# Performance work log

Measured on AMD Instinct MI355X. Metric: run time of the kernel, lower is better.

The kernel has to match this reference:

```python
import jax, jax.numpy as jnp
import numpy as np

N, E, IN_DIM, H, OUT, MAPD = 20000, 640000, 24, 128, 24, 512
SLOPE = 0.01  # torch F.leaky_relu default


def setup_inputs() -> dict:
    key = jax.random.key(0)
    ks = jax.random.split(key, 20)
    g = lambda i, shape, s: jax.random.normal(ks[i], shape, jnp.float32) * s
    inp = {
        "feats": g(0, (N, IN_DIM), 1.0),
        "e_w": jax.random.uniform(ks[1], (E, 1), dtype=jnp.float32),
        "maps_embedding": g(2, (N, MAPD), 1.0),
        "snorm_n": jnp.ones((N, 1), jnp.float32),
        "src": jax.random.randint(ks[3], (E,), 0, N),
        "dst": jax.random.randint(ks[4], (E,), 0, N),
        "W_eh": g(5, (H, IN_DIM), (2.0 / IN_DIM) ** 0.5), "b_eh": jnp.zeros((H,), jnp.float32),
        "W_ee": g(6, (H, 1), 1.0), "b_ee": jnp.zeros((H,), jnp.float32),
        "W_cat": g(7, (H, H + MAPD), (2.0 / (H + MAPD)) ** 0.5), "b_cat": jnp.zeros((H,), jnp.float32),
        "Ws1": g(8, (H, H), (2.0 / H) ** 0.5), "Wf1": g(9, (H, H), (2.0 / H) ** 0.5),
        "a1": g(10, (2 * H,), (2.0 / (2 * H)) ** 0.5),
        "Ws2": g(11, (H, H), (2.0 / H) ** 0.5), "Wf2": g(12, (H, H), (2.0 / H) ** 0.5),
        "a2": g(13, (2 * H,), (2.0 / (2 * H)) ** 0.5),
        "W_out": g(14, (OUT, H), (2.0 / H) ** 0.5), "b_out": jnp.zeros((OUT,), jnp.float32),
    }
    return inp


def gat_layer(h, src, dst, Ws, Wf, a):
    # My_GATLayer with (as constructed in My_GAT) relu=False, att_ew=False, dropouts=0.
    h_in = h
    h_s = h @ Ws.T                         # [N,H] self transform
    z = h @ Wf.T                           # [N,H] message transform
    # attention score = leaky_relu(a^T [z_src, z_dst]) computed via per-node halves
    s_src = z @ a[:H]                      # [N]
    s_dst = z @ a[H:]                      # [N]
    e = jax.nn.leaky_relu(s_src[src] + s_dst[dst], SLOPE)          # [E]
    # numerically stable segment softmax over incoming edges grouped by dst
    m = jax.ops.segment_max(e, dst, num_segments=N)
    m = jnp.where(jnp.isfinite(m), m, 0.0)
    ex = jnp.exp(e - m[dst])
    denom = jax.ops.segment_sum(ex, dst, num_segments=N)
    alpha = ex / jnp.maximum(denom[dst], 1e-16)                    # [E]
    agg = jax.ops.segment_sum(alpha[:, None] * z[src], dst, num_segments=N)  # [N,H]
    indeg = jax.ops.segment_sum(jnp.ones_like(e), dst, num_segments=N)
    # DGL update_all leaves zero-in-degree nodes at their prior ndata['h'] (= h_in)
    h_node = jnp.where(indeg[:, None] > 0, h_s + agg, h_in)
    return h_in + h_node                   # residual connection; relu disabled (positional-arg bug)


def reference(feats, e_w, maps_embedding, snorm_n, src, dst,
              W_eh, b_eh, W_ee, b_ee, W_cat, b_cat,
              Ws1, Wf1, a1, Ws2, Wf2, a2, W_out, b_out):
    feats = feats.reshape(feats.shape[0], -1)
    h = feats @ W_eh.T + b_eh                                  # embedding_h
    _e = e_w @ W_ee.T + b_ee                                   # edge embedding (stored on g.edata['w'], unused since att_ew binds to attn_drop)
    h = jnp.concatenate([maps_embedding, h], axis=-1) @ W_cat.T + b_cat
    h = jax.nn.relu(h)
    h = gat_layer(h, src, dst, Ws1, Wf1, a1)
    h = gat_layer(h, src, dst, Ws2, Wf2, a2)
    return h @ W_out.T + b_out
```

## Files before the change

kernel.cpp:

```cpp
#include <hip/hip_runtime.h>

#define HBLK 128
#define EPB 4096

typedef __attribute__((ext_vector_type(8))) short s8v;
typedef __attribute__((ext_vector_type(4))) float f32x4;
typedef __attribute__((ext_vector_type(8))) _Float16 h8f;

__device__ inline void split2(float x, short& h, short& l) {
    unsigned hb = __float_as_uint(x) & 0xFFFF0000u;
    float hf = __uint_as_float(hb);
    float lf = x - hf;
    h = (short)(hb >> 16);
    l = (short)(__float_as_uint(lf) >> 16);
}

__device__ inline void split8(const float4& a0, const float4& a1, s8v& ah, s8v& al) {
    float vv[8];
    *(float4*)&vv[0] = a0;
    *(float4*)&vv[4] = a1;
#pragma unroll
    for (int e = 0; e < 8; ++e) {
        short hh, ll;
        split2(vv[e], hh, ll);
        ah[e] = hh;
        al[e] = ll;
    }
}


__global__ void hist_pack(const int* __restrict__ dst, int* __restrict__ histT,
                          int E, int NB1,
                          const float* __restrict__ W0, const float* __restrict__ W1,
                          const float* __restrict__ W2, const float* __restrict__ W3,
                          short* __restrict__ dh, short* __restrict__ dl,
                          const float* __restrict__ Wcat, int ldw, int mapd,
                          const float* __restrict__ Weh, int indim,
                          const float* __restrict__ beh, const float* __restrict__ bcat,
                          short* __restrict__ ch,
                          float* __restrict__ bcomb, int K) {
    __shared__ int h[256];
    const int y = blockIdx.y;
    const int t = threadIdx.x;
    if (y == 0) {
        const int blk = blockIdx.x;
        if (blk >= NB1) return;
        h[t] = 0;
        __syncthreads();
        const int e0 = blk * EPB;
        const int e1 = min(E, e0 + EPB);
        for (int e = e0 + t; e < e1; e += 256)
            atomicAdd(&h[dst[e] >> 7], 1);
        __syncthreads();
        histT[t * NB1 + blk] = h[t];
    } else if (y < 5) {
        if (blockIdx.x >= 64) return;
        const int m = y - 1;
        const long i = (long)blockIdx.x * 256 + t;
        const float* Ws[4] = {W0, W1, W2, W3};
        const int c = (int)(i >> 7), k = (int)(i & 127);
        float x = Ws[m][c * HBLK + k];
        short hh, ll;
        split2(x, hh, ll);
        const int j = c >> 4, l16 = c & 15;
        const int chunk = k >> 5, quad = (k >> 3) & 3, tt = k & 7;
        const long off = (long)m * 16384 + (((long)(chunk * 8 + j) * 64) + quad * 16 + l16) * 8 + tt;
        dh[off] = hh;
        dl[off] = ll;
    } else {
        const long i = (long)blockIdx.x * 256 + t;
        const long total = (long)HBLK * K;
        if (i < total) {
            const int c = (int)(i / K), k = (int)(i % K);
            float x = 0.f;
            if (k < mapd) {
                x = Wcat[(long)c * ldw + k];
            } else if (k < mapd + indim) {
                const float* wc = Wcat + (long)c * ldw + mapd;
                const int kk = k - mapd;
                float s = 0.f;
                for (int j = 0; j < HBLK; ++j) s += wc[j] * Weh[j * indim + kk];
                x = s;
            }
            short hh, ll;
            split2(x, hh, ll);
            const int j = c >> 4, l16 = c & 15;
            const int chunk = k >> 5, quad = (k >> 3) & 3, tt = k & 7;
            const long off = (((long)(chunk * 8 + j) * 64) + quad * 16 + l16) * 8 + tt;
            ch[off] = hh;
        } else if (i < total + HBLK) {
            const int c = (int)(i - total);
            const float* wc = Wcat + (long)c * ldw + mapd;
            float s = bcat[c];
            for (int j = 0; j < HBLK; ++j) s += wc[j] * beh[j];
            bcomb[c] = s;
        }
    }
}

__global__ void scan1(const int* __restrict__ counts, int* __restrict__ offs,
                      int* __restrict__ bsums, int n) {
    __shared__ int lds[256];
    const int t = threadIdx.x;
    const int i = blockIdx.x * 256 + t;
    const int v = (i < n) ? counts[i] : 0;
    lds[t] = v;
    __syncthreads();
    for (int off = 1; off < 256; off <<= 1) {
        int add = (t >= off) ? lds[t - off] : 0;
        __syncthreads();
        lds[t] += add;
        __syncthreads();
    }
    if (i < n) offs[i] = lds[t] - v;
    if (t == 255) bsums[blockIdx.x] = lds[255];
}

__device__ inline void local_bsum_scan(const int* __restrict__ bsums, int nb,
                                       int* bex, int* tmp) {
    const int t = threadIdx.x;
    const int v = (t < nb) ? bsums[t] : 0;
    tmp[t] = v;
    __syncthreads();
    for (int off = 1; off < 256; off <<= 1) {
        int add = (t >= off) ? tmp[t - off] : 0;
        __syncthreads();
        tmp[t] += add;
        __syncthreads();
    }
    bex[t] = tmp[t] - v;
    __syncthreads();
}

__global__ void bin_scatter(const int* __restrict__ src, const int* __restrict__ dst,
                            const int* __restrict__ histT, const int* __restrict__ bsums,
                            int* __restrict__ ebuf, int E, int NB1) {
    __shared__ int cur[256];
    __shared__ int bex[256];
    __shared__ int tmp[256];
    const int t = threadIdx.x, blk = blockIdx.x;
    local_bsum_scan(bsums, NB1, bex, tmp);
    const int li = t * NB1 + blk;
    cur[t] = histT[li] + bex[li >> 8];
    __syncthreads();
    const int e0 = blk * EPB;
    const int e1 = min(E, e0 + EPB);
    for (int e = e0 + t; e < e1; e += 256) {
        const int d = dst[e];
        const int p = atomicAdd(&cur[d >> 7], 1);
        ebuf[p] = (src[e] << 7) | (d & 127);
    }
}

__global__ void bucket_sort(const int* __restrict__ ebuf, const int* __restrict__ histT,
                            const int* __restrict__ bsums,
                            int* __restrict__ offs, int* __restrict__ srcs,
                            int N, int E, int NB1) {
    __shared__ int cnt[256];
    __shared__ int cur[256];
    __shared__ int bex[256];
    const int t = threadIdx.x, b = blockIdx.x;
    local_bsum_scan(bsums, NB1, bex, cnt);
    const int li0 = b * NB1;
    const int ebase = histT[li0] + bex[li0 >> 8];
    int eend = E;
    if (b + 1 < 256) {
        const int li1 = (b + 1) * NB1;
        eend = histT[li1] + bex[li1 >> 8];
    }
    cnt[t] = 0;
    __syncthreads();
    for (int e = ebase + t; e < eend; e += 256)
        atomicAdd(&cnt[ebuf[e] & 127], 1);
    __syncthreads();
    const int own = cnt[t];
    for (int off = 1; off < 256; off <<= 1) {
        int add = (t >= off) ? cnt[t - off] : 0;
        __syncthreads();
        cnt[t] += add;
        __syncthreads();
    }
    const int excl = cnt[t] - own;
    cur[t] = ebase + excl;
    const int node = (b << 7) + t;
    if (t < 128 && node < N) offs[node] = ebase + excl;
    if (b == 0 && t == 0) offs[N] = E;
    __syncthreads();
    for (int e = ebase + t; e < eend; e += 256) {
        const int ed = ebuf[e];
        const int p = atomicAdd(&cur[ed & 127], 1);
        srcs[p] = ed >> 7;
    }
}

__global__ __launch_bounds__(128, 2) void gemm_bigk(
    const float* __restrict__ A1, int lda1, int K1,
    const float* __restrict__ A2, int lda2, int Kin,
    int K,
    const short* __restrict__ Wh,
    const float* __restrict__ bias,
    float* __restrict__ Cf, int M)
{
    __shared__ short lds_h[2][4096];
    const int tid = threadIdx.x;
    const int wv = tid >> 6;
    const int lane = tid & 63;
    const int l16 = lane & 15;
    const int quad = lane >> 4;
    const int m0 = blockIdx.x * 32 + wv * 16;
    int ra = m0 + l16;
    if (ra >= M) ra = M - 1;
    const long r1 = (long)ra * lda1;
    const long r2 = (long)ra * lda2;
    const int NC = K >> 5;

    f32x4 acc[8];
#pragma unroll
    for (int j = 0; j < 8; ++j) acc[j] = (f32x4){0.f, 0.f, 0.f, 0.f};

#define LOAD_A(d0, d1, kb)                                      \
    {                                                           \
        const int col0 = (kb) + quad * 8;                       \
        if (col0 < K1) {                                        \
            const float* ap = A1 + r1 + col0;                   \
            d0 = *(const float4*)ap;                            \
            d1 = *(const float4*)(ap + 4);                      \
        } else if (col0 < Kin) {                                \
            const float* ap = A2 + r2 + (col0 - K1);            \
            d0 = *(const float4*)ap;                            \
            d1 = *(const float4*)(ap + 4);                      \
        } else {                                                \
            d0 = make_float4(0.f, 0.f, 0.f, 0.f);               \
            d1 = make_float4(0.f, 0.f, 0.f, 0.f);               \
        }                                                       \
    }
#define LOAD_W(c)                                               \
    {                                                           \
        const int4* gh = (const int4*)(Wh + (long)(c) * 4096);  \
        wh0 = gh[tid * 4];     wh1 = gh[tid * 4 + 1];           \
        wh2 = gh[tid * 4 + 2]; wh3 = gh[tid * 4 + 3];           \
    }
#define WRITE_W(b)                                              \
    {                                                           \
        int4* bh = (int4*)lds_h[b];                             \
        bh[tid * 4] = wh0;     bh[tid * 4 + 1] = wh1;           \
        bh[tid * 4 + 2] = wh2; bh[tid * 4 + 3] = wh3;           \
    }

    int4 wh0, wh1, wh2, wh3;
    LOAD_W(0)
    WRITE_W(0)
    LOAD_W(1)
    float4 a0c, a1c, a0n, a1n, a0p, a1p;
    float4 a0q = make_float4(0.f, 0.f, 0.f, 0.f);
    float4 a1q = make_float4(0.f, 0.f, 0.f, 0.f);
    LOAD_A(a0c, a1c, 0)
    LOAD_A(a0n, a1n, 32)
    LOAD_A(a0p, a1p, 64)
    asm volatile("s_waitcnt lgkmcnt(0)" ::: "memory");
    __builtin_amdgcn_s_barrier();
    asm volatile("" ::: "memory");

    for (int c = 0; c < NC; ++c) {
        const int nb = c & 1;
        if (c + 3 < NC) {
            LOAD_A(a0q, a1q, (c + 3) * 32)
        }
        s8v ah, al;
        split8(a0c, a1c, ah, al);
#pragma unroll
        for (int j = 0; j < 8; ++j) {
            const s8v whf = *(const s8v*)&lds_h[nb][(j * 64 + lane) * 8];
            acc[j] = __builtin_amdgcn_mfma_f32_16x16x32_bf16(ah, whf, acc[j], 0, 0, 0);
            acc[j] = __builtin_amdgcn_mfma_f32_16x16x32_bf16(al, whf, acc[j], 0, 0, 0);
        }
        if (c + 1 < NC) {
            WRITE_W(nb ^ 1)
            if (c + 2 < NC) LOAD_W(c + 2)
            asm volatile("s_waitcnt lgkmcnt(0)" ::: "memory");
            __builtin_amdgcn_s_barrier();
            asm volatile("" ::: "memory");
        }
        a0c = a0n; a1c = a1n;
        a0n = a0p; a1n = a1p;
        a0p = a0q; a1p = a1q;
    }
#undef LOAD_A
#undef LOAD_W
#undef WRITE_W

#pragma unroll
    for (int r = 0; r < 4; ++r) {
        const int gr = m0 + quad * 4 + r;
        if (gr >= M) continue;
#pragma unroll
        for (int j = 0; j < 8; ++j) {
            const int col = j * 16 + l16;
            float v = acc[j][r] + bias[col];
            Cf[(long)gr * HBLK + col] = fmaxf(v, 0.f);
        }
    }
}

__global__ __launch_bounds__(256, 2) void gemm_layer(
    const float* __restrict__ A,
    const short* __restrict__ Wsh,
    const short* __restrict__ Wfh, const short* __restrict__ Wfl,
    float* __restrict__ hsOut, _Float16* __restrict__ zOut,
    const float* __restrict__ avec,
    float* __restrict__ sOut, float* __restrict__ dOut, int M)
{
    __shared__ short lh[16384];
    __shared__ short ll[16384];
    const int tid = threadIdx.x;
    const int wv = tid >> 6;
    const int lane = tid & 63;
    const int l16 = lane & 15;
    const int quad = lane >> 4;
    const int m0 = blockIdx.x * 64 + wv * 16;
    int ra = m0 + l16;
    if (ra >= M) ra = M - 1;
    const float* arow = A + (long)ra * HBLK + quad * 8;

    {
        const int4* gh = (const int4*)Wfh;
        const int4* gl = (const int4*)Wfl;
        int4* bh = (int4*)lh;
        int4* bl = (int4*)ll;
#pragma unroll
        for (int i = 0; i < 8; ++i) {
            bh[i * 256 + tid] = gh[i * 256 + tid];
            bl[i * 256 + tid] = gl[i * 256 + tid];
        }
    }
    float4 aw0[4], aw1[4];
#pragma unroll
    for (int c = 0; c < 4; ++c) {
        aw0[c] = *(const float4*)(arow + c * 32);
        aw1[c] = *(const float4*)(arow + c * 32 + 4);
    }
    int4 wsh[8];
    {
        const int4* gh = (const int4*)Wsh;
#pragma unroll
        for (int i = 0; i < 8; ++i) wsh[i] = gh[i * 256 + tid];
    }
    s8v ahf[4], alf[4];
#pragma unroll
    for (int c = 0; c < 4; ++c) split8(aw0[c], aw1[c], ahf[c], alf[c]);

    f32x4 acc[8];
#pragma unroll
    for (int j = 0; j < 8; ++j) acc[j] = (f32x4){0.f, 0.f, 0.f, 0.f};
    asm volatile("s_waitcnt lgkmcnt(0)" ::: "memory");
    __builtin_amdgcn_s_barrier();
    asm volatile("" ::: "memory");

#pragma unroll
    for (int c = 0; c < 4; ++c) {
#pragma unroll
        for (int j = 0; j < 8; ++j) {
            const s8v whf = *(const s8v*)&lh[((c * 8 + j) * 64 + lane) * 8];
            const s8v wlf = *(const s8v*)&ll[((c * 8 + j) * 64 + lane) * 8];
            acc[j] = __builtin_amdgcn_mfma_f32_16x16x32_bf16(ahf[c], whf, acc[j], 0, 0, 0);
            acc[j] = __builtin_amdgcn_mfma_f32_16x16x32_bf16(ahf[c], wlf, acc[j], 0, 0, 0);
            acc[j] = __builtin_amdgcn_mfma_f32_16x16x32_bf16(alf[c], whf, acc[j], 0, 0, 0);
        }
    }
#pragma unroll
    for (int r = 0; r < 4; ++r) {
        const int gr = m0 + quad * 4 + r;
        if (gr >= M) continue;
#pragma unroll
        for (int j = 0; j < 8; ++j)
            zOut[(long)gr * HBLK + j * 16 + l16] = (_Float16)acc[j][r];
    }
    {
        float av0[8], av1[8];
#pragma unroll
        for (int j = 0; j < 8; ++j) {
            av0[j] = avec[j * 16 + l16];
            av1[j] = avec[128 + j * 16 + l16];
        }
#pragma unroll
        for (int r = 0; r < 4; ++r) {
            float ssp = 0.f, sdp = 0.f;
#pragma unroll
            for (int j = 0; j < 8; ++j) {
                const float v = acc[j][r];
                ssp += v * av0[j];
                sdp += v * av1[j];
            }
#pragma unroll
            for (int off = 1; off < 16; off <<= 1) {
                ssp += __shfl_xor(ssp, off);
                sdp += __shfl_xor(sdp, off);
            }
            const int gr = m0 + quad * 4 + r;
            if (l16 == 0 && gr < M) {
                sOut[gr] = ssp;
                dOut[gr] = sdp;
            }
        }
    }

    asm volatile("s_waitcnt lgkmcnt(0)" ::: "memory");
    __builtin_amdgcn_s_barrier();
    asm volatile("" ::: "memory");
    {
        int4* bh = (int4*)lh;
#pragma unroll
        for (int i = 0; i < 8; ++i) bh[i * 256 + tid] = wsh[i];
    }
    asm volatile("s_waitcnt lgkmcnt(0)" ::: "memory");
    __builtin_amdgcn_s_barrier();
    asm volatile("" ::: "memory");

#pragma unroll
    for (int j = 0; j < 8; ++j) acc[j] = (f32x4){0.f, 0.f, 0.f, 0.f};
#pragma unroll
    for (int c = 0; c < 4; ++c) {
#pragma unroll
        for (int j = 0; j < 8; ++j) {
            const s8v whf = *(const s8v*)&lh[((c * 8 + j) * 64 + lane) * 8];
            acc[j] = __builtin_amdgcn_mfma_f32_16x16x32_bf16(ahf[c], whf, acc[j], 0, 0, 0);
            acc[j] = __builtin_amdgcn_mfma_f32_16x16x32_bf16(alf[c], whf, acc[j], 0, 0, 0);
        }
    }
#pragma unroll
    for (int r = 0; r < 4; ++r) {
        const int gr = m0 + quad * 4 + r;
        if (gr >= M) continue;
#pragma unroll
        for (int j = 0; j < 8; ++j)
            hsOut[(long)gr * HBLK + j * 16 + l16] = acc[j][r];
    }
}

template <int FOUT>
__global__ void gat_gather(const float* __restrict__ h_in, const float* __restrict__ hs,
                           const _Float16* __restrict__ zh,
                           const float* __restrict__ s_src, const float* __restrict__ s_dst,
                           const int* __restrict__ offs, const int* __restrict__ srcs,
                           float* __restrict__ h_out,
                           const float* __restrict__ Wout, const float* __restrict__ bout,
                           float* __restrict__ outp, int OUTD, int N) {
    __shared__ float wlds[FOUT ? (32 * 132 + 4 * 132) : 4];
    const int tid = threadIdx.x;
    const int wave = tid >> 6;
    const int lane = tid & 63;
    if constexpr (FOUT) {
        for (int i = tid; i < OUTD * HBLK; i += 256)
            wlds[(i >> 7) * 132 + (i & 127)] = Wout[i];
        __syncthreads();
    }
    const int n = blockIdx.x * 4 + wave;
    if (n >= N) return;
    const int g = lane >> 4, l = lane & 15;
    const int beg = offs[n], end = offs[n + 1];
    const int deg = end - beg;
    const float sd = s_dst[n];

    const long base = (long)n * HBLK + 8 * l;
    float4 hi0, hi1, hv0, hv1;
    if (g == 0) {
        hi0 = *(const float4*)(h_in + base);
        hi1 = *(const float4*)(h_in + base + 4);
        if (deg > 0) {
            hv0 = *(const float4*)(hs + base);
            hv1 = *(const float4*)(hs + base + 4);
        }
    }
    float bo = 0.f;
    if constexpr (FOUT) {
        if (lane < OUTD) bo = bout[lane];
    }

    float acc[8] = {};
    if (deg > 0) {
        if (deg <= 64) {
            const int sA = srcs[beg + min(lane, deg - 1)];
            float e = sd + s_src[sA];
            e = e > 0.f ? e : 0.01f * e;
            if (lane >= deg) e = -INFINITY;
            float mv = e;
#pragma unroll
            for (int off = 32; off; off >>= 1) mv = fmaxf(mv, __shfl_xor(mv, off));
            const float ex = (lane < deg) ? __expf(e - mv) : 0.f;
            float sv = ex;
#pragma unroll
            for (int off = 32; off; off >>= 1) sv += __shfl_xor(sv, off);
            const float w = ex / fmaxf(sv, 1e-16f);

            const int nK = (deg + 3) >> 2;
            int k = 0;
            for (; k + 1 < nK; k += 2) {
                const int i0 = 4 * k + g;
                const int i1 = i0 + 4;
                const int s0 = __shfl(sA, i0);
                const int s1 = __shfl(sA, i1);
                const float w0 = __shfl(w, i0);
                const float w1 = __shfl(w, i1);
                const h8f z0 = *(const h8f*)(zh + (long)s0 * HBLK + 8 * l);
                const h8f z1 = *(const h8f*)(zh + (long)s1 * HBLK + 8 * l);
#pragma unroll
                for (int e2 = 0; e2 < 8; ++e2)
                    acc[e2] += w0 * (float)z0[e2] + w1 * (float)z1[e2];
            }
            if (k < nK) {
                const int i0 = 4 * k + g;
                const int s0 = __shfl(sA, i0);
                const float w0 = __shfl(w, i0);
                const h8f z0 = *(const h8f*)(zh + (long)s0 * HBLK + 8 * l);
#pragma unroll
                for (int e2 = 0; e2 < 8; ++e2)
                    acc[e2] += w0 * (float)z0[e2];
            }
        } else {
            float m = -INFINITY, s = 0.f;
            for (int i = beg + lane; i < end; i += 64) {
                float e = sd + s_src[srcs[i]];
                e = e > 0.f ? e : 0.01f * e;
                float nm = fmaxf(m, e);
                s = s * __expf(m - nm) + __expf(e - nm);
                m = nm;
            }
#pragma unroll
            for (int off = 32; off > 0; off >>= 1) {
                float m2 = __shfl_down(m, off);
                float s2 = __shfl_down(s, off);
                if (m2 > m) {
                    float t = m; m = m2; m2 = t;
                    float ts = s; s = s2; s2 = ts;
                }
                s = (m == -INFINITY) ? 0.f : s + s2 * __expf(m2 - m);
            }
            m = __shfl(m, 0);
            s = __shfl(s, 0);
            const float inv = 1.f / fmaxf(s, 1e-16f);
            for (int i = beg + g; i < end; i += 4) {
                const int s0 = srcs[i];
                float e0 = sd + s_src[s0];
                e0 = e0 > 0.f ? e0 : 0.01f * e0;
                const float w0 = __expf(e0 - m) * inv;
                const h8f z0 = *(const h8f*)(zh + (long)s0 * HBLK + 8 * l);
#pragma unroll
                for (int e2 = 0; e2 < 8; ++e2)
                    acc[e2] += w0 * (float)z0[e2];
            }
        }
#pragma unroll
        for (int e2 = 0; e2 < 8; ++e2) {
            acc[e2] += __shfl_down(acc[e2], 32);
            acc[e2] += __shfl_down(acc[e2], 16);
        }
    }

    if (g == 0) {
        float o[8];
        if (deg > 0) {
            const float* hip = (const float*)&hi0;
            const float* hvp = (const float*)&hv0;
#pragma unroll
            for (int e = 0; e < 4; ++e) o[e] = hip[e] + hvp[e] + acc[e];
            const float* hip1 = (const float*)&hi1;
            const float* hvp1 = (const float*)&hv1;
#pragma unroll
            for (int e = 0; e < 4; ++e) o[4 + e] = hip1[e] + hvp1[e] + acc[4 + e];
        } else {
            const float* hip = (const float*)&hi0;
            const float* hip1 = (const float*)&hi1;
#pragma unroll
            for (int e = 0; e < 4; ++e) o[e] = 2.f * hip[e];
#pragma unroll
            for (int e = 0; e < 4; ++e) o[4 + e] = 2.f * hip1[e];
        }
        if constexpr (FOUT) {
            float* hr = wlds + 32 * 132 + wave * 132;
            *(float4*)&hr[8 * l] = *(float4*)&o[0];
            *(float4*)&hr[8 * l + 4] = *(float4*)&o[4];
        } else {
            *(float4*)(h_out + base) = *(float4*)&o[0];
            *(float4*)(h_out + base + 4) = *(float4*)&o[4];
        }
    }
    if constexpr (FOUT) {
        if (lane < OUTD) {
            const float* hr = wlds + 32 * 132 + wave * 132;
            const float* wr = wlds + lane * 132;
            float a = bo;
#pragma unroll 8
            for (int k = 0; k < 32; ++k) {
                const float4 hv = *(const float4*)&hr[k * 4];
                const float4 wv = *(const float4*)&wr[k * 4];
                a += hv.x * wv.x + hv.y * wv.y + hv.z * wv.z + hv.w * wv.w;
            }
            outp[(long)n * OUTD + lane] = a;
        }
    }
}

extern "C" void kernel_launch(void* const* d_in, const int* in_sizes, int n_in,
                              void* d_out, int out_size, void* d_ws, size_t ws_size,
                              hipStream_t stream) {
    const float* feats = (const float*)d_in[0];
    const float* maps  = (const float*)d_in[2];
    const int* src = (const int*)d_in[4];
    const int* dst = (const int*)d_in[5];
    const float* W_eh  = (const float*)d_in[6];
    const float* b_eh  = (const float*)d_in[7];
    const float* W_cat = (const float*)d_in[10];
    const float* b_cat = (const float*)d_in[11];
    const float* Ws1 = (const float*)d_in[12];
    const float* Wf1 = (const float*)d_in[13];
    const float* a1  = (const float*)d_in[14];
    const float* Ws2 = (const float*)d_in[15];
    const float* Wf2 = (const float*)d_in[16];
    const float* a2  = (const float*)d_in[17];
    const float* W_out = (const float*)d_in[18];
    const float* b_out = (const float*)d_in[19];

    const int N = in_sizes[3];
    const int E = in_sizes[4];
    const int IN_DIM = in_sizes[0] / N;
    const int MAPD = in_sizes[2] / N;
    const int OUTD = in_sizes[19];
    const int KCAT = MAPD + HBLK;
    const int KC = (MAPD + IN_DIM + 31) & ~31;

    char* p = (char*)d_ws;
    const size_t NH = (size_t)N * HBLK;
    float* hin  = (float*)p;  p += NH * 4;
    float* hs   = (float*)p;  p += NH * 4;
    float* hout = (float*)p;  p += NH * 4;
    _Float16* zh = (_Float16*)p; p += NH * 2;
    float* ssrc = (float*)p;  p += (size_t)N * 4;
    float* sdst = (float*)p;  p += (size_t)N * 4;
    int* offs   = (int*)p;    p += (size_t)(N + 1) * 4;
    int* srcs   = (int*)p;    p += (size_t)E * 4;
    int* bsums  = (int*)p;    p += 256 * 4;
    int* histT  = (int*)p;    p += (size_t)256 * 256 * 4;
    float* bcomb = (float*)p; p += (size_t)HBLK * 4;
    p = (char*)(((uintptr_t)p + 15) & ~(uintptr_t)15);
    int* ebuf = (int*)p;      p += (size_t)E * 4;
    short* Wcat_h = (short*)p; p += (size_t)HBLK * KC * 2;
    short* Wly_h = (short*)p;  p += (size_t)4 * HBLK * HBLK * 2;
    short* Wly_l = (short*)p;  p += (size_t)4 * HBLK * HBLK * 2;

    const int NB1 = (E + EPB - 1) / EPB;
    const int NBUCK = (N + 127) >> 7;
    const int nHist = 256 * NB1;
    const int nbW = (HBLK * KC + HBLK + 255) / 256;
    const int gx = (nbW > NB1) ? nbW : NB1;
    hist_pack<<<dim3(gx, 6), 256, 0, stream>>>(
        dst, histT, E, NB1,
        Ws1, Wf1, Ws2, Wf2, Wly_h, Wly_l,
        W_cat, KCAT, MAPD, W_eh, IN_DIM, b_eh, b_cat, Wcat_h, bcomb, KC);
    scan1<<<NB1, 256, 0, stream>>>(histT, histT, bsums, nHist);
    bin_scatter<<<NB1, 256, 0, stream>>>(src, dst, histT, bsums, ebuf, E, NB1);
    bucket_sort<<<NBUCK, 256, 0, stream>>>(ebuf, histT, bsums, offs, srcs, N, E, NB1);

    const int gGridB = (N + 31) / 32;
    const int gGrid = (N + 63) / 64;
    const int n4 = (N + 3) / 4;

    gemm_bigk<<<gGridB, 128, 0, stream>>>(
        maps, MAPD, MAPD, feats, IN_DIM, MAPD + IN_DIM, KC,
        Wcat_h, bcomb, hin, N);

    gemm_layer<<<gGrid, 256, 0, stream>>>(
        hin, Wly_h, Wly_h + 16384, Wly_l + 16384,
        hs, zh, a1, ssrc, sdst, N);
    gat_gather<0><<<n4, 256, 0, stream>>>(hin, hs, zh, ssrc, sdst, offs, srcs, hout,
                                          nullptr, nullptr, nullptr, OUTD, N);

    gemm_layer<<<gGrid, 256, 0, stream>>>(
        hout, Wly_h + 32768, Wly_h + 49152, Wly_l + 49152,
        hs, zh, a2, ssrc, sdst, N);
    gat_gather<1><<<n4, 256, 0, stream>>>(hout, hs, zh, ssrc, sdst, offs, srcs, nullptr,
                                          W_out, b_out, (float*)d_out, OUTD, N);
}
```

Measured before the change: 247.2 us.

## Fold histogram scan into scatter kernels and load GEMM weights directly to registers

Drops the separate scan1 kernel. Each bin_scatter and bucket_sort block now recomputes the row sums of the histogram and their prefix scan itself, which saves a launch at the cost of redundant reads of the histogram. gemm_bigk changes to single-wave blocks of 16 rows. Each wave loads its bf16 weight fragments straight from global memory into double-buffered registers instead of staging them through LDS with barriers. This removes LDS traffic and synchronisation but makes every wave reload the full weight matrix and raises register pressure.

New measurement: 274.3 us. 10.9% more time.

```diff
diff --git a/kernel.cpp b/kernel.cpp
--- a/kernel.cpp
+++ b/kernel.cpp
@@ -98,29 +98,20 @@
     }
 }
 
-__global__ void scan1(const int* __restrict__ counts, int* __restrict__ offs,
-                      int* __restrict__ bsums, int n) {
-    __shared__ int lds[256];
-    const int t = threadIdx.x;
-    const int i = blockIdx.x * 256 + t;
-    const int v = (i < n) ? counts[i] : 0;
-    lds[t] = v;
-    __syncthreads();
-    for (int off = 1; off < 256; off <<= 1) {
-        int add = (t >= off) ? lds[t - off] : 0;
-        __syncthreads();
-        lds[t] += add;
-        __syncthreads();
-    }
-    if (i < n) offs[i] = lds[t] - v;
-    if (t == 255) bsums[blockIdx.x] = lds[255];
-}
-
-__device__ inline void local_bsum_scan(const int* __restrict__ bsums, int nb,
-                                       int* bex, int* tmp) {
-    const int t = threadIdx.x;
-    const int v = (t < nb) ? bsums[t] : 0;
-    tmp[t] = v;
+__global__ void bin_scatter(const int* __restrict__ src, const int* __restrict__ dst,
+                            const int* __restrict__ histT,
+                            int* __restrict__ ebuf, int E, int NB1) {
+    __shared__ int cur[256];
+    __shared__ int tmp[256];
+    const int t = threadIdx.x, blk = blockIdx.x;
+    int rowsum = 0, part = 0;
+    const int* row = histT + t * NB1;
+    for (int b2 = 0; b2 < NB1; ++b2) {
+        const int v = row[b2];
+        rowsum += v;
+        part += (b2 < blk) ? v : 0;
+    }
+    tmp[t] = rowsum;
     __syncthreads();
     for (int off = 1; off < 256; off <<= 1) {
         int add = (t >= off) ? tmp[t - off] : 0;
@@ -128,20 +119,7 @@
         tmp[t] += add;
         __syncthreads();
     }
-    bex[t] = tmp[t] - v;
-    __syncthreads();
-}
-
-__global__ void bin_scatter(const int* __restrict__ src, const int* __restrict__ dst,
-                            const int* __restrict__ histT, const int* __restrict__ bsums,
-                            int* __restrict__ ebuf, int E, int NB1) {
-    __shared__ int cur[256];
-    __shared__ int bex[256];
-    __shared__ int tmp[256];
-    const int t = threadIdx.x, blk = blockIdx.x;
-    local_bsum_scan(bsums, NB1, bex, tmp);
-    const int li = t * NB1 + blk;
-    cur[t] = histT[li] + bex[li >> 8];
+    cur[t] = (tmp[t] - rowsum) + part;
     __syncthreads();
     const int e0 = blk * EPB;
     const int e1 = min(E, e0 + EPB);
@@ -153,21 +131,29 @@
 }
 
 __global__ void bucket_sort(const int* __restrict__ ebuf, const int* __restrict__ histT,
-                            const int* __restrict__ bsums,
                             int* __restrict__ offs, int* __restrict__ srcs,
                             int N, int E, int NB1) {
     __shared__ int cnt[256];
     __shared__ int cur[256];
-    __shared__ int bex[256];
+    __shared__ int bexs[256];
+    __shared__ int sums[256];
     const int t = threadIdx.x, b = blockIdx.x;
-    local_bsum_scan(bsums, NB1, bex, cnt);
-    const int li0 = b * NB1;
-    const int ebase = histT[li0] + bex[li0 >> 8];
-    int eend = E;
-    if (b + 1 < 256) {
-        const int li1 = (b + 1) * NB1;
-        eend = histT[li1] + bex[li1 >> 8];
-    }
+    int rowsum = 0;
+    const int* row = histT + t * NB1;
+    for (int b2 = 0; b2 < NB1; ++b2) rowsum += row[b2];
+    cnt[t] = rowsum;
+    __syncthreads();
+    for (int off = 1; off < 256; off <<= 1) {
+        int add = (t >= off) ? cnt[t - off] : 0;
+        __syncthreads();
+        cnt[t] += add;
+        __syncthreads();
+    }
+    bexs[t] = cnt[t] - rowsum;
+    sums[t] = rowsum;
+    __syncthreads();
+    const int ebase = bexs[b];
+    const int eend = bexs[b] + sums[b];
     cnt[t] = 0;
     __syncthreads();
     for (int e = ebase + t; e < eend; e += 256)
@@ -193,7 +179,7 @@
     }
 }
 
-__global__ __launch_bounds__(128, 2) void gemm_bigk(
+__global__ __launch_bounds__(64) void gemm_bigk(
     const float* __restrict__ A1, int lda1, int K1,
     const float* __restrict__ A2, int lda2, int Kin,
     int K,
@@ -201,13 +187,10 @@
     const float* __restrict__ bias,
     float* __restrict__ Cf, int M)
 {
-    __shared__ short lds_h[2][4096];
-    const int tid = threadIdx.x;
-    const int wv = tid >> 6;
-    const int lane = tid & 63;
+    const int lane = threadIdx.x;
     const int l16 = lane & 15;
     const int quad = lane >> 4;
-    const int m0 = blockIdx.x * 32 + wv * 16;
+    const int m0 = blockIdx.x * 16;
     int ra = m0 + l16;
     if (ra >= M) ra = M - 1;
     const long r1 = (long)ra * lda1;
@@ -234,60 +217,48 @@
             d1 = make_float4(0.f, 0.f, 0.f, 0.f);               \
         }                                                       \
     }
-#define LOAD_W(c)                                               \
-    {                                                           \
-        const int4* gh = (const int4*)(Wh + (long)(c) * 4096);  \
-        wh0 = gh[tid * 4];     wh1 = gh[tid * 4 + 1];           \
-        wh2 = gh[tid * 4 + 2]; wh3 = gh[tid * 4 + 3];           \
-    }
-#define WRITE_W(b)                                              \
-    {                                                           \
-        int4* bh = (int4*)lds_h[b];                             \
-        bh[tid * 4] = wh0;     bh[tid * 4 + 1] = wh1;           \
-        bh[tid * 4 + 2] = wh2; bh[tid * 4 + 3] = wh3;           \
-    }
-
-    int4 wh0, wh1, wh2, wh3;
-    LOAD_W(0)
-    WRITE_W(0)
-    LOAD_W(1)
+#define LOAD_WF(dstw, c)                                                         \
+    {                                                                            \
+        _Pragma("unroll")                                                        \
+        for (int j = 0; j < 8; ++j)                                              \
+            dstw[j] = *(const s8v*)(Wh + (((long)(c) * 8 + j) * 64 + lane) * 8); \
+    }
+#define COMPUTE(a0, a1, wreg)                                                    \
+    {                                                                            \
+        s8v ah, al;                                                              \
+        split8(a0, a1, ah, al);                                                  \
+        _Pragma("unroll")                                                        \
+        for (int j = 0; j < 8; ++j) {                                            \
+            acc[j] = __builtin_amdgcn_mfma_f32_16x16x32_bf16(ah, wreg[j], acc[j], 0, 0, 0); \
+            acc[j] = __builtin_amdgcn_mfma_f32_16x16x32_bf16(al, wreg[j], acc[j], 0, 0, 0); \
+        }                                                                        \
+    }
+
+    s8v wA[8], wB[8];
+    LOAD_WF(wA, 0)
+    if (1 < NC) LOAD_WF(wB, 1)
     float4 a0c, a1c, a0n, a1n, a0p, a1p;
-    float4 a0q = make_float4(0.f, 0.f, 0.f, 0.f);
-    float4 a1q = make_float4(0.f, 0.f, 0.f, 0.f);
     LOAD_A(a0c, a1c, 0)
     LOAD_A(a0n, a1n, 32)
     LOAD_A(a0p, a1p, 64)
-    asm volatile("s_waitcnt lgkmcnt(0)" ::: "memory");
-    __builtin_amdgcn_s_barrier();
-    asm volatile("" ::: "memory");
-
-    for (int c = 0; c < NC; ++c) {
-        const int nb = c & 1;
-        if (c + 3 < NC) {
-            LOAD_A(a0q, a1q, (c + 3) * 32)
-        }
-        s8v ah, al;
-        split8(a0c, a1c, ah, al);
-#pragma unroll
-        for (int j = 0; j < 8; ++j) {
-            const s8v whf = *(const s8v*)&lds_h[nb][(j * 64 + lane) * 8];
-            acc[j] = __builtin_amdgcn_mfma_f32_16x16x32_bf16(ah, whf, acc[j], 0, 0, 0);
-            acc[j] = __builtin_amdgcn_mfma_f32_16x16x32_bf16(al, whf, acc[j], 0, 0, 0);
-        }
-        if (c + 1 < NC) {
-            WRITE_W(nb ^ 1)
-            if (c + 2 < NC) LOAD_W(c + 2)
-            asm volatile("s_waitcnt lgkmcnt(0)" ::: "memory");
-            __builtin_amdgcn_s_barrier();
-            asm volatile("" ::: "memory");
-        }
+
+    for (int c = 0; c < NC; c += 2) {
+        COMPUTE(a0c, a1c, wA)
+        if (c + 2 < NC) LOAD_WF(wA, c + 2)
         a0c = a0n; a1c = a1n;
         a0n = a0p; a1n = a1p;
-        a0p = a0q; a1p = a1q;
+        if (c + 3 < NC) LOAD_A(a0p, a1p, (c + 3) * 32)
+        if (c + 1 < NC) {
+            COMPUTE(a0c, a1c, wB)
+            if (c + 3 < NC) LOAD_WF(wB, c + 3)
+            a0c = a0n; a1c = a1n;
+            a0n = a0p; a1n = a1p;
+            if (c + 4 < NC) LOAD_A(a0p, a1p, (c + 4) * 32)
+        }
     }
 #undef LOAD_A
-#undef LOAD_W
-#undef WRITE_W
+#undef LOAD_WF
+#undef COMPUTE
 
 #pragma unroll
     for (int r = 0; r < 4; ++r) {
@@ -638,7 +609,6 @@
     float* sdst = (float*)p;  p += (size_t)N * 4;
     int* offs   = (int*)p;    p += (size_t)(N + 1) * 4;
     int* srcs   = (int*)p;    p += (size_t)E * 4;
-    int* bsums  = (int*)p;    p += 256 * 4;
     int* histT  = (int*)p;    p += (size_t)256 * 256 * 4;
     float* bcomb = (float*)p; p += (size_t)HBLK * 4;
     p = (char*)(((uintptr_t)p + 15) & ~(uintptr_t)15);
@@ -649,22 +619,20 @@
 
     const int NB1 = (E + EPB - 1) / EPB;
     const int NBUCK = (N + 127) >> 7;
-    const int nHist = 256 * NB1;
     const int nbW = (HBLK * KC + HBLK + 255) / 256;
     const int gx = (nbW > NB1) ? nbW : NB1;
     hist_pack<<<dim3(gx, 6), 256, 0, stream>>>(
         dst, histT, E, NB1,
         Ws1, Wf1, Ws2, Wf2, Wly_h, Wly_l,
         W_cat, KCAT, MAPD, W_eh, IN_DIM, b_eh, b_cat, Wcat_h, bcomb, KC);
-    scan1<<<NB1, 256, 0, stream>>>(histT, histT, bsums, nHist);
-    bin_scatter<<<NB1, 256, 0, stream>>>(src, dst, histT, bsums, ebuf, E, NB1);
-    bucket_sort<<<NBUCK, 256, 0, stream>>>(ebuf, histT, bsums, offs, srcs, N, E, NB1);
-
-    const int gGridB = (N + 31) / 32;
+    bin_scatter<<<NB1, 256, 0, stream>>>(src, dst, histT, ebuf, E, NB1);
+    bucket_sort<<<NBUCK, 256, 0, stream>>>(ebuf, histT, offs, srcs, N, E, NB1);
+
+    const int gGridB = (N + 15) / 16;
     const int gGrid = (N + 63) / 64;
     const int n4 = (N + 3) / 4;
 
-    gemm_bigk<<<gGridB, 128, 0, stream>>>(
+    gemm_bigk<<<gGridB, 64, 0, stream>>>(
         maps, MAPD, MAPD, feats, IN_DIM, MAPD + IN_DIM, KC,
         Wcat_h, bcomb, hin, N);
 
```
